# Performance work log

Measured on AMD Instinct MI355X. Metric: run time of the kernel, lower is better.

Reference implementation:

```python
import jax, jax.numpy as jnp
import numpy as np

L = 4      # num_decoders
D = 512    # d (model dim)
F = 512    # f (attention dim; must equal D for residual adds)
V = 32000  # vocab_size
S = 2048   # sequence length
EPS = 1e-5


def layer_norm(x, g, b):
    mu = jnp.mean(x, axis=-1, keepdims=True)
    var = jnp.var(x, axis=-1, keepdims=True)
    return (x - mu) * jax.lax.rsqrt(var + EPS) * g + b


def setup_inputs() -> dict:
    key = jax.random.key(0)
    ks = jax.random.split(key, 20)
    s = 0.02
    n = jax.random.normal
    return {
        "x":   n(ks[0], (S, D), jnp.float32),
        "Wq":  n(ks[1], (L, D, F), jnp.float32) * s,
        "bq":  jnp.zeros((L, F), jnp.float32),
        "Wk":  n(ks[2], (L, D, F), jnp.float32) * s,
        "bk":  jnp.zeros((L, F), jnp.float32),
        "Wv":  n(ks[3], (L, D, F), jnp.float32) * s,
        "bv":  jnp.zeros((L, F), jnp.float32),
        "Wp":  n(ks[4], (L, F, F), jnp.float32) * s,
        "bp":  jnp.zeros((L, F), jnp.float32),
        "g1":  1.0 + n(ks[5], (L, F), jnp.float32) * s,
        "be1": n(ks[6], (L, F), jnp.float32) * s,
        "W1":  n(ks[7], (L, F, 4 * F), jnp.float32) * s,
        "b1":  jnp.zeros((L, 4 * F), jnp.float32),
        "W2":  n(ks[8], (L, 4 * F, D), jnp.float32) * s,
        "b2":  jnp.zeros((L, D), jnp.float32),
        "g2":  1.0 + n(ks[9], (L, D), jnp.float32) * s,
        "be2": n(ks[10], (L, D), jnp.float32) * s,
        "Wf":  n(ks[11], (D, V), jnp.float32) * s,
        "bf":  jnp.zeros((V,), jnp.float32),
    }


def reference(x, Wq, bq, Wk, bk, Wv, bv, Wp, bp, g1, be1, W1, b1, W2, b2, g2, be2, Wf, bf):
    seq = x.shape[0]
    scale = 1.0 / jnp.sqrt(jnp.asarray(F, x.dtype))
    # causal mask: position i attends to j <= i (intended triu masking)
    causal = jnp.tril(jnp.ones((seq, seq), dtype=bool))
    neg_inf = jnp.asarray(-jnp.inf, x.dtype)
    for l in range(L):
        res = jax.lax.stop_gradient(x)  # original uses x.detach().clone()
        q = x @ Wq[l] + bq[l]
        k = x @ Wk[l] + bk[l]
        v = x @ Wv[l] + bv[l]
        scores = (q @ k.T) * scale                      # [S, S]
        scores = jnp.where(causal, scores, neg_inf)
        att = jax.nn.softmax(scores, axis=1)
        z = (att @ v) @ Wp[l] + bp[l]
        x = layer_norm(z + res, g1[l], be1[l])
        res = jax.lax.stop_gradient(x)
        h = x @ W1[l] + b1[l]                           # no activation in original FFN
        h = h @ W2[l] + b2[l]
        x = layer_norm(h + res, g2[l], be2[l])
    logits = x @ Wf + bf                                # [S, V]
    return jax.nn.softmax(logits, axis=1)
```

## Files before the change

kernel.cpp:

```cpp
#include <hip/hip_runtime.h>
#include <cmath>

#define SEQ 2048
#define DIM 512
#define FDIM 512
#define HDIM 2048
#define VOCAB 32000
#define NLAYER 4
#define LNEPS 1e-5f

typedef unsigned short ushort_t;
typedef __attribute__((ext_vector_type(8))) short short8;
typedef __attribute__((ext_vector_type(4))) float f32x4;

__device__ __forceinline__ ushort_t f2bf(float x) {
    union { float f; unsigned int u; } a; a.f = x;
    unsigned int r = a.u + 0x7fffu + ((a.u >> 16) & 1u);
    return (ushort_t)(r >> 16);
}
__device__ __forceinline__ float bf2f(ushort_t b) {
    union { unsigned int u; float f; } a; a.u = ((unsigned int)b) << 16; return a.f;
}

__device__ __forceinline__ void gload_lds16(const ushort_t* g, ushort_t* l) {
    __builtin_amdgcn_global_load_lds(
        (const __attribute__((address_space(1))) void*)g,
        (__attribute__((address_space(3))) void*)l, 16, 0, 0);
}

#define GEMM_CORE(AH, AL, BH, BL, LDA, LDB, KSTEPS, KBASE)                         \
    __shared__ ushort_t lds[16384];                                                \
    ushort_t* ldsAh = lds;                                                         \
    ushort_t* ldsAl = lds + 4096;                                                  \
    ushort_t* ldsBh = lds + 8192;                                                  \
    ushort_t* ldsBl = lds + 12288;                                                 \
    const int tid  = threadIdx.x;                                                  \
    const int lane = tid & 63, wv = tid >> 6;                                      \
    const int wm = wv >> 1, wn = wv & 1;                                           \
    const int q = lane >> 4, mlo = lane & 15;                                      \
    const int tm = blockIdx.y << 7, tn = blockIdx.x << 7;                          \
    f32x4 acc[4][4];                                                               \
    _Pragma("unroll")                                                              \
    for (int i = 0; i < 4; i++)                                                    \
        _Pragma("unroll")                                                          \
        for (int j = 0; j < 4; j++)                                                \
            acc[i][j] = (f32x4){0.f, 0.f, 0.f, 0.f};                               \
    for (int ks = 0; ks < (KSTEPS); ks++) {                                        \
        const int k0 = (KBASE) + (ks << 5);                                        \
        _Pragma("unroll")                                                          \
        for (int r = 0; r < 2; r++) {                                              \
            const int c  = (r << 8) + (wv << 6) + lane;                            \
            const int i  = c & 127, kb = c >> 7;                                   \
            const int lofs = ((r << 8) + (wv << 6)) << 3;                          \
            const size_t aoff = (size_t)(tm + i) * (LDA) + k0 + (kb << 3);         \
            const size_t boff = (size_t)(tn + i) * (LDB) + k0 + (kb << 3);         \
            gload_lds16((AH) + aoff, ldsAh + lofs);                                \
            gload_lds16((AL) + aoff, ldsAl + lofs);                                \
            gload_lds16((BH) + boff, ldsBh + lofs);                                \
            gload_lds16((BL) + boff, ldsBl + lofs);                                \
        }                                                                          \
        __syncthreads();                                                           \
        short8 ah[4], al[4], bh[4], bl[4];                                         \
        _Pragma("unroll")                                                          \
        for (int t = 0; t < 4; t++) {                                              \
            const int ma = ((q << 7) + (wm << 6) + (t << 4) + mlo) << 3;           \
            const int nb = ((q << 7) + (wn << 6) + (t << 4) + mlo) << 3;           \
            ah[t] = *(const short8*)&ldsAh[ma];                                    \
            al[t] = *(const short8*)&ldsAl[ma];                                    \
            bh[t] = *(const short8*)&ldsBh[nb];                                    \
            bl[t] = *(const short8*)&ldsBl[nb];                                    \
        }                                                                          \
        _Pragma("unroll")                                                          \
        for (int i = 0; i < 4; i++)                                                \
            _Pragma("unroll")                                                      \
            for (int j = 0; j < 4; j++) {                                          \
                acc[i][j] = __builtin_amdgcn_mfma_f32_16x16x32_bf16(ah[i], bh[j], acc[i][j], 0, 0, 0); \
                acc[i][j] = __builtin_amdgcn_mfma_f32_16x16x32_bf16(ah[i], bl[j], acc[i][j], 0, 0, 0); \
                acc[i][j] = __builtin_amdgcn_mfma_f32_16x16x32_bf16(al[i], bh[j], acc[i][j], 0, 0, 0); \
            }                                                                      \
        __syncthreads();                                                           \
    }

__global__ __launch_bounds__(256) void gemm_bf16x3_k(
    const ushort_t* __restrict__ Ah, const ushort_t* __restrict__ Al,
    const ushort_t* __restrict__ Bh, const ushort_t* __restrict__ Bl,
    const float* __restrict__ bias, float* __restrict__ C,
    int K, int lda, int ldb, int ldc, float scale, int splitk, int flags,
    int bsA, int bsB, int bsC, int bsBias)
{
    const int bz = blockIdx.z;
    const int l  = bz / splitk, zz = bz - l * splitk;
    Ah += (size_t)l * bsA; Al += (size_t)l * bsA;
    Bh += (size_t)l * bsB; Bl += (size_t)l * bsB;
    C  += (size_t)l * bsC;
    if (bias != nullptr) bias += (size_t)l * bsBias;
    const int tmq = blockIdx.y << 7, tnq = blockIdx.x << 7;
    if ((flags & 1) && tnq > tmq + 127) return;
    int ksteps = (K >> 5) / splitk;
    const int kbase = zz * ksteps * 32;
    if (flags & 2) {
        const int rem = (tmq + 128 - kbase) >> 5;
        if (rem < ksteps) ksteps = rem;
        if (ksteps <= 0) return;
    }
    GEMM_CORE(Ah, Al, Bh, Bl, lda, ldb, ksteps, kbase)
    const bool addb = (bias != nullptr) && (zz == 0);
#pragma unroll
    for (int ti = 0; ti < 4; ti++)
#pragma unroll
        for (int tj = 0; tj < 4; tj++) {
            const int col = tn + (wn << 6) + (tj << 4) + mlo;
            const float bb = addb ? bias[col] : 0.f;
#pragma unroll
            for (int r = 0; r < 4; r++) {
                const int row = tm + (wm << 6) + (ti << 4) + (q << 2) + r;
                const float v = acc[ti][tj][r] * scale + bb;
                if (splitk == 1) C[(size_t)row * ldc + col] = v;
                else atomicAdd(&C[(size_t)row * ldc + col], v);
            }
        }
}

__global__ __launch_bounds__(256) void gemm_bf16x3_sp_k(
    const ushort_t* __restrict__ Ah, const ushort_t* __restrict__ Al,
    const ushort_t* __restrict__ Bh, const ushort_t* __restrict__ Bl,
    const float* __restrict__ bias,
    ushort_t* __restrict__ Dh, ushort_t* __restrict__ Dl,
    int K, int lda, int ldb, int ldo)
{
    GEMM_CORE(Ah, Al, Bh, Bl, lda, ldb, (K >> 5), 0)
#pragma unroll
    for (int ti = 0; ti < 4; ti++)
#pragma unroll
        for (int tj = 0; tj < 4; tj++) {
            const int col = tn + (wn << 6) + (tj << 4) + mlo;
            const float bb = (bias != nullptr) ? bias[col] : 0.f;
#pragma unroll
            for (int r = 0; r < 4; r++) {
                const int row = tm + (wm << 6) + (ti << 4) + (q << 2) + r;
                const float v = acc[ti][tj][r] + bb;
                const ushort_t h = f2bf(v);
                Dh[(size_t)row * ldo + col] = h;
                Dl[(size_t)row * ldo + col] = f2bf(v - bf2f(h));
            }
        }
}

__global__ __launch_bounds__(128) void split_k(
    const float* __restrict__ src, int ld, int C,
    ushort_t* __restrict__ dh, ushort_t* __restrict__ dl)
{
    const int row = blockIdx.y;
    const int c4 = ((blockIdx.x << 7) + threadIdx.x) << 2;
    if (c4 >= C) return;
    const float4 v = *(const float4*)&src[(size_t)row * ld + c4];
    ushort_t h[4], l[4];
    const float f[4] = {v.x, v.y, v.z, v.w};
#pragma unroll
    for (int i = 0; i < 4; i++) {
        h[i] = f2bf(f[i]);
        l[i] = f2bf(f[i] - bf2f(h[i]));
    }
    *(ushort4*)&dh[(size_t)row * C + c4] = make_ushort4(h[0], h[1], h[2], h[3]);
    *(ushort4*)&dl[(size_t)row * C + c4] = make_ushort4(l[0], l[1], l[2], l[3]);
}

__global__ __launch_bounds__(256) void tsplit_k(
    const float* __restrict__ src, int ld, int R,
    ushort_t* __restrict__ dh, ushort_t* __restrict__ dl)
{
    __shared__ float t[32][33];
    const int c = threadIdx.x & 31, r8 = threadIdx.x >> 5;
    const int bx = blockIdx.x, by = blockIdx.y;
#pragma unroll
    for (int i = 0; i < 4; i++) {
        const int r = (r8 << 2) + i;
        t[r][c] = src[(size_t)((by << 5) + r) * ld + (bx << 5) + c];
    }
    __syncthreads();
#pragma unroll
    for (int i = 0; i < 4; i++) {
        const int rr = (r8 << 2) + i;
        const float v = t[c][rr];
        const ushort_t h = f2bf(v);
        const ushort_t l = f2bf(v - bf2f(h));
        const size_t o = (size_t)((bx << 5) + rr) * R + (by << 5) + c;
        dh[o] = h; dl[o] = l;
    }
}

__global__ __launch_bounds__(256) void tsplit_b_k(
    const float* __restrict__ src0, int ld, int R, int sbs,
    ushort_t* __restrict__ dh0, ushort_t* __restrict__ dl0, int dbs)
{
    const int lz = blockIdx.z;
    const float* src = src0 + (size_t)lz * sbs;
    ushort_t* dh = dh0 + (size_t)lz * dbs;
    ushort_t* dl = dl0 + (size_t)lz * dbs;
    __shared__ float t[32][33];
    const int c = threadIdx.x & 31, r8 = threadIdx.x >> 5;
    const int bx = blockIdx.x, by = blockIdx.y;
#pragma unroll
    for (int i = 0; i < 4; i++) {
        const int r = (r8 << 2) + i;
        t[r][c] = src[(size_t)((by << 5) + r) * ld + (bx << 5) + c];
    }
    __syncthreads();
#pragma unroll
    for (int i = 0; i < 4; i++) {
        const int rr = (r8 << 2) + i;
        const float v = t[c][rr];
        const ushort_t h = f2bf(v);
        const ushort_t l = f2bf(v - bf2f(h));
        const size_t o = (size_t)((bx << 5) + rr) * R + (by << 5) + c;
        dh[o] = h; dl[o] = l;
    }
}

__global__ void gatherqkv_k(const float* bq, const float* bk, const float* bv, float* d)
{
    const int i = blockIdx.x * 256 + threadIdx.x;
    if (i >= NLAYER * 1536) return;
    const int l = i / 1536, j = i - l * 1536;
    float v;
    if (j < 512)       v = bq[l * 512 + j];
    else if (j < 1024) v = bk[l * 512 + j - 512];
    else               v = bv[l * 512 + j - 1024];
    d[i] = v;
}

__global__ __launch_bounds__(256) void bvec_k(
    const float* __restrict__ b1, const float* __restrict__ W2,
    float* __restrict__ bv)
{
    const int lz = blockIdx.z;
    b1 += (size_t)lz * HDIM;
    W2 += (size_t)lz * HDIM * DIM;
    bv += (size_t)lz * DIM;
    const int c  = (blockIdx.x << 7) + (threadIdx.x & 127);
    const int h0 = (blockIdx.y << 7) + (threadIdx.x >> 7);
    float acc = 0.f;
#pragma unroll 8
    for (int i = 0; i < 64; i++) {
        const int h = h0 + (i << 1);
        acc += b1[h] * W2[(size_t)h * DIM + c];
    }
    atomicAdd(&bv[c], acc);
}

__global__ __launch_bounds__(256) void softmax_causal_split_k(
    const float* __restrict__ sc, ushort_t* __restrict__ dh, ushort_t* __restrict__ dl)
{
    const int i = blockIdx.x;
    const float* row = sc + (size_t)i * SEQ;
    const int tid = threadIdx.x;
    __shared__ float red[4];
    const int base = tid << 2;

    float4 v[2];
    v[0] = *(const float4*)&row[base];
    v[1] = *(const float4*)&row[1024 + base];

    float m = -3.402823466e38f;
#pragma unroll
    for (int c = 0; c < 2; c++) {
        float* f = (float*)&v[c];
        const int idx = (c << 10) + base;
#pragma unroll
        for (int j = 0; j < 4; j++) {
            if (idx + j > i) f[j] = -3.402823466e38f;
            m = fmaxf(m, f[j]);
        }
    }
#pragma unroll
    for (int o = 32; o > 0; o >>= 1) m = fmaxf(m, __shfl_down(m, o, 64));
    if ((tid & 63) == 0) red[tid >> 6] = m;
    __syncthreads();
    m = fmaxf(fmaxf(red[0], red[1]), fmaxf(red[2], red[3]));
    __syncthreads();

    float s = 0.f;
#pragma unroll
    for (int c = 0; c < 2; c++) {
        float* f = (float*)&v[c];
#pragma unroll
        for (int j = 0; j < 4; j++) {
            f[j] = expf(f[j] - m);
            s += f[j];
        }
    }
#pragma unroll
    for (int o = 32; o > 0; o >>= 1) s += __shfl_down(s, o, 64);
    if ((tid & 63) == 0) red[tid >> 6] = s;
    __syncthreads();
    const float inv = 1.0f / (red[0] + red[1] + red[2] + red[3]);

#pragma unroll
    for (int c = 0; c < 2; c++) {
        float* f = (float*)&v[c];
        const int idx = (c << 10) + base;
        ushort_t hp[4], lp[4];
#pragma unroll
        for (int j = 0; j < 4; j++) {
            const float e = f[j] * inv;
            hp[j] = f2bf(e);
            lp[j] = f2bf(e - bf2f(hp[j]));
        }
        *(ushort4*)&dh[(size_t)i * SEQ + idx] = make_ushort4(hp[0], hp[1], hp[2], hp[3]);
        *(ushort4*)&dl[(size_t)i * SEQ + idx] = make_ushort4(lp[0], lp[1], lp[2], lp[3]);
    }
}

__global__ __launch_bounds__(256) void add_ln_split_k(
    const float* __restrict__ z, const float* __restrict__ res,
    const float* __restrict__ g, const float* __restrict__ b,
    float* __restrict__ outp, ushort_t* __restrict__ dh, ushort_t* __restrict__ dl)
{
    const int row = blockIdx.x;
    const int tid = threadIdx.x;
    __shared__ float red[4];
    const size_t base = (size_t)row * DIM;
    const float v0 = z[base + tid] + res[base + tid];
    const float v1 = z[base + tid + 256] + res[base + tid + 256];
    float s = v0 + v1;
#pragma unroll
    for (int o = 32; o > 0; o >>= 1) s += __shfl_down(s, o, 64);
    if ((tid & 63) == 0) red[tid >> 6] = s;
    __syncthreads();
    const float mean = (red[0] + red[1] + red[2] + red[3]) * (1.0f / DIM);
    __syncthreads();
    const float d0 = v0 - mean, d1 = v1 - mean;
    float vs = d0 * d0 + d1 * d1;
#pragma unroll
    for (int o = 32; o > 0; o >>= 1) vs += __shfl_down(vs, o, 64);
    if ((tid & 63) == 0) red[tid >> 6] = vs;
    __syncthreads();
    const float var = (red[0] + red[1] + red[2] + red[3]) * (1.0f / DIM);
    const float inv = 1.0f / sqrtf(var + LNEPS);
    const float o0 = d0 * inv * g[tid] + b[tid];
    const float o1 = d1 * inv * g[tid + 256] + b[tid + 256];
    outp[base + tid]       = o0;
    outp[base + tid + 256] = o1;
    const ushort_t h0 = f2bf(o0), h1 = f2bf(o1);
    dh[base + tid]       = h0;  dl[base + tid]       = f2bf(o0 - bf2f(h0));
    dh[base + tid + 256] = h1;  dl[base + tid + 256] = f2bf(o1 - bf2f(h1));
}

__global__ __launch_bounds__(1024) void softmax_rows_k(float* __restrict__ p)
{
    const int row = blockIdx.x;
    float* r = p + (size_t)row * VOCAB;
    const int tid = threadIdx.x;
    __shared__ float red[16];
    const int base = tid << 2;

    float4 v[8];
#pragma unroll
    for (int c = 0; c < 7; c++) v[c] = *(const float4*)&r[(c << 12) + base];
    const bool tail = (28672 + base) < VOCAB;
    if (tail) v[7] = *(const float4*)&r[28672 + base];
    else { v[7].x = v[7].y = v[7].z = v[7].w = -3.402823466e38f; }

    float m = -3.402823466e38f;
#pragma unroll
    for (int c = 0; c < 8; c++)
        m = fmaxf(m, fmaxf(fmaxf(v[c].x, v[c].y), fmaxf(v[c].z, v[c].w)));
#pragma unroll
    for (int o = 32; o > 0; o >>= 1) m = fmaxf(m, __shfl_down(m, o, 64));
    if ((tid & 63) == 0) red[tid >> 6] = m;
    __syncthreads();
    m = red[0];
#pragma unroll
    for (int w = 1; w < 16; w++) m = fmaxf(m, red[w]);
    __syncthreads();

    float s = 0.f;
#pragma unroll
    for (int c = 0; c < 8; c++) {
        float* f = (float*)&v[c];
#pragma unroll
        for (int j = 0; j < 4; j++) {
            f[j] = expf(f[j] - m);
            s += f[j];
        }
    }
#pragma unroll
    for (int o = 32; o > 0; o >>= 1) s += __shfl_down(s, o, 64);
    if ((tid & 63) == 0) red[tid >> 6] = s;
    __syncthreads();
    float tot = 0.f;
#pragma unroll
    for (int w = 0; w < 16; w++) tot += red[w];
    const float inv = 1.0f / tot;

#pragma unroll
    for (int c = 0; c < 7; c++) {
        float4 o4;
        o4.x = v[c].x * inv; o4.y = v[c].y * inv;
        o4.z = v[c].z * inv; o4.w = v[c].w * inv;
        *(float4*)&r[(c << 12) + base] = o4;
    }
    if (tail) {
        float4 o4;
        o4.x = v[7].x * inv; o4.y = v[7].y * inv;
        o4.z = v[7].z * inv; o4.w = v[7].w * inv;
        *(float4*)&r[28672 + base] = o4;
    }
}

extern "C" void kernel_launch(void* const* d_in, const int* in_sizes, int n_in,
                              void* d_out, int out_size, void* d_ws, size_t ws_size,
                              hipStream_t stream)
{
    const float* x   = (const float*)d_in[0];
    const float* Wq  = (const float*)d_in[1];
    const float* bq  = (const float*)d_in[2];
    const float* Wk  = (const float*)d_in[3];
    const float* bk  = (const float*)d_in[4];
    const float* Wv  = (const float*)d_in[5];
    const float* bv  = (const float*)d_in[6];
    const float* Wp  = (const float*)d_in[7];
    const float* bp  = (const float*)d_in[8];
    const float* g1  = (const float*)d_in[9];
    const float* be1 = (const float*)d_in[10];
    const float* W1  = (const float*)d_in[11];
    const float* b1  = (const float*)d_in[12];
    const float* W2  = (const float*)d_in[13];
    const float* b2  = (const float*)d_in[14];
    const float* g2  = (const float*)d_in[15];
    const float* be2 = (const float*)d_in[16];
    const float* Wf  = (const float*)d_in[17];
    const float* bf  = (const float*)d_in[18];
    float* out = (float*)d_out;

    char* ws = (char*)d_ws;
    auto alloc = [&](size_t bytes) {
        void* p = ws;
        ws += (bytes + 255) & ~(size_t)255;
        return p;
    };
    float*    x0     = (float*)alloc((size_t)SEQ * DIM * 4);
    float*    x1     = (float*)alloc((size_t)SEQ * DIM * 4);
    float*    vp     = (float*)alloc((size_t)SEQ * FDIM * 4);
    float*    z2     = (float*)alloc((size_t)SEQ * FDIM * 4);
    float*    sc     = (float*)alloc((size_t)SEQ * SEQ * 4);
    float*    PtA    = (float*)alloc((size_t)NLAYER * FDIM * DIM * 4);
    ushort_t* QKVh   = (ushort_t*)alloc((size_t)SEQ * 1536 * 2);
    ushort_t* QKVl   = (ushort_t*)alloc((size_t)SEQ * 1536 * 2);
    ushort_t* X0h    = (ushort_t*)alloc((size_t)SEQ * DIM * 2);
    ushort_t* X0l    = (ushort_t*)alloc((size_t)SEQ * DIM * 2);
    ushort_t* X1h    = (ushort_t*)alloc((size_t)SEQ * DIM * 2);
    ushort_t* X1l    = (ushort_t*)alloc((size_t)SEQ * DIM * 2);
    ushort_t* AttH   = (ushort_t*)alloc((size_t)SEQ * SEQ * 2);
    ushort_t* AttL   = (ushort_t*)alloc((size_t)SEQ * SEQ * 2);
    ushort_t* Wbh    = (ushort_t*)alloc((size_t)NLAYER * 1536 * 512 * 2);
    ushort_t* Wbl    = (ushort_t*)alloc((size_t)NLAYER * 1536 * 512 * 2);
    ushort_t* WpTh   = (ushort_t*)alloc((size_t)NLAYER * 512 * 512 * 2);
    ushort_t* WpTl   = (ushort_t*)alloc((size_t)NLAYER * 512 * 512 * 2);
    ushort_t* W2th   = (ushort_t*)alloc((size_t)NLAYER * 512 * 2048 * 2);
    ushort_t* W2tl   = (ushort_t*)alloc((size_t)NLAYER * 512 * 2048 * 2);
    ushort_t* W1h    = (ushort_t*)alloc((size_t)NLAYER * 512 * 2048 * 2);
    ushort_t* W1l    = (ushort_t*)alloc((size_t)NLAYER * 512 * 2048 * 2);
    ushort_t* Pth    = (ushort_t*)alloc((size_t)NLAYER * 512 * 512 * 2);
    ushort_t* Ptl    = (ushort_t*)alloc((size_t)NLAYER * 512 * 512 * 2);
    ushort_t* VpTh   = (ushort_t*)alloc((size_t)FDIM * SEQ * 2);
    ushort_t* VpTl   = (ushort_t*)alloc((size_t)FDIM * SEQ * 2);
    ushort_t* Wfh    = (ushort_t*)alloc((size_t)VOCAB * DIM * 2);
    ushort_t* Wfl    = (ushort_t*)alloc((size_t)VOCAB * DIM * 2);
    float*    bqkvA  = (float*)alloc((size_t)NLAYER * 1536 * 4);
    float*    bvecA  = (float*)alloc((size_t)NLAYER * DIM * 4);

    const float att_scale = 1.0f / sqrtf((float)FDIM);
    const dim3 b256(256), b128(128), b1024(1024);

    auto split = [&](const float* src, int ld, int R, int C, ushort_t* dh, ushort_t* dl) {
        split_k<<<dim3((C / 4 + 127) / 128, R), b128, 0, stream>>>(src, ld, C, dh, dl);
    };
    auto gemm = [&](const ushort_t* ah, const ushort_t* al,
                    const ushort_t* bh, const ushort_t* bl,
                    const float* bias, float* C, int M, int N, int K,
                    int lda, int ldb, int ldc, float scale, int splitk, int flags) {
        if (splitk > 1)
            hipMemsetAsync(C, 0, (size_t)M * ldc * 4, stream);
        gemm_bf16x3_k<<<dim3(N / 128, M / 128, splitk), b256, 0, stream>>>(
            ah, al, bh, bl, bias, C, K, lda, ldb, ldc, scale, splitk, flags, 0, 0, 0, 0);
    };

    hipMemcpyAsync(x0, x, (size_t)SEQ * DIM * 4, hipMemcpyDeviceToDevice, stream);
    tsplit_b_k<<<dim3(16, 16, NLAYER), b256, 0, stream>>>(Wq, FDIM, DIM, 262144, Wbh, Wbl, 786432);
    tsplit_b_k<<<dim3(16, 16, NLAYER), b256, 0, stream>>>(Wk, FDIM, DIM, 262144, Wbh + 262144, Wbl + 262144, 786432);
    tsplit_b_k<<<dim3(16, 16, NLAYER), b256, 0, stream>>>(Wv, FDIM, DIM, 262144, Wbh + 524288, Wbl + 524288, 786432);
    tsplit_b_k<<<dim3(16, 16, NLAYER), b256, 0, stream>>>(Wp, FDIM, FDIM, 262144, WpTh, WpTl, 262144);
    tsplit_b_k<<<dim3(16, 64, NLAYER), b256, 0, stream>>>(W2, DIM, HDIM, HDIM * DIM, W2th, W2tl, 1048576);
    split(W1, HDIM, NLAYER * FDIM, HDIM, W1h, W1l);
    hipMemsetAsync(PtA, 0, (size_t)NLAYER * FDIM * DIM * 4, stream);
    gemm_bf16x3_k<<<dim3(4, 4, NLAYER * 8), b256, 0, stream>>>(
        W2th, W2tl, W1h, W1l, nullptr, PtA, HDIM, HDIM, HDIM, DIM, 1.0f, 8, 0,
        1048576, 1048576, 262144, 0);
    split(PtA, DIM, NLAYER * FDIM, DIM, Pth, Ptl);
    gatherqkv_k<<<dim3((NLAYER * 1536 + 255) / 256), b256, 0, stream>>>(bq, bk, bv, bqkvA);
    hipMemcpyAsync(bvecA, b2, (size_t)NLAYER * DIM * 4, hipMemcpyDeviceToDevice, stream);
    bvec_k<<<dim3(4, 16, NLAYER), b256, 0, stream>>>(b1, W2, bvecA);
    tsplit_k<<<dim3(VOCAB / 32, DIM / 32), b256, 0, stream>>>(Wf, VOCAB, DIM, Wfh, Wfl);
    split(x0, DIM, SEQ, DIM, X0h, X0l);

    for (int l = 0; l < NLAYER; l++) {
        gemm_bf16x3_sp_k<<<dim3(12, 16), b256, 0, stream>>>(
            X0h, X0l, Wbh + (size_t)l * 786432, Wbl + (size_t)l * 786432,
            bqkvA + (size_t)l * 1536, QKVh, QKVl, DIM, DIM, DIM, 1536);

        gemm(QKVh + 1024, QKVl + 1024, WpTh + (size_t)l * 262144, WpTl + (size_t)l * 262144,
             nullptr, vp, SEQ, FDIM, FDIM, 1536, FDIM, FDIM, 1.0f, 4, 0);

        gemm(QKVh, QKVl, QKVh + 512, QKVl + 512, nullptr, sc,
             SEQ, SEQ, FDIM, 1536, 1536, SEQ, att_scale, 2, 1);
        softmax_causal_split_k<<<dim3(SEQ), b256, 0, stream>>>(sc, AttH, AttL);

        tsplit_k<<<dim3(16, 64), b256, 0, stream>>>(vp, FDIM, SEQ, VpTh, VpTl);
        gemm(AttH, AttL, VpTh, VpTl, bp + l * FDIM, z2,
             SEQ, FDIM, SEQ, SEQ, SEQ, FDIM, 1.0f, 4, 2);

        add_ln_split_k<<<dim3(SEQ), b256, 0, stream>>>(
            z2, x0, g1 + l * FDIM, be1 + l * FDIM, x1, X1h, X1l);

        gemm(X1h, X1l, Pth + (size_t)l * 262144, Ptl + (size_t)l * 262144,
             bvecA + (size_t)l * DIM, z2, SEQ, DIM, FDIM, DIM, DIM, DIM, 1.0f, 4, 0);

        add_ln_split_k<<<dim3(SEQ), b256, 0, stream>>>(
            z2, x1, g2 + l * DIM, be2 + l * DIM, x0, X0h, X0l);
    }

    gemm_bf16x3_k<<<dim3(VOCAB / 128, SEQ / 128, 1), b256, 0, stream>>>(
        X0h, X0l, Wfh, Wfl, bf, out, DIM, DIM, DIM, VOCAB, 1.0f, 1, 0, 0, 0, 0, 0);
    softmax_rows_k<<<dim3(SEQ), b1024, 0, stream>>>(out);
}
```

Baseline: 1.687 ms.

## Fold Wv into Wp, replace atomic split-K with partial buffers, swizzle vocab GEMM

Precomputes Wv·Wp (and bv·Wp) once, so the V projection goes straight into a transposed layout. This removes the per-layer vp GEMM and the transpose-split kernel. Split-K GEMMs now write separate partial buffers that the softmax and add+layernorm kernels sum, which drops the memsets and atomics. Partial sums that are causally empty are skipped. Softmax stores only the columns inside the causal limit, and the final vocab GEMM swaps block indices so consecutive blocks share weight tiles. The cost is more memory traffic for the partial buffers and a slightly different rounding order.

After: 1.514 ms. 10.3% less time.

```diff
diff --git a/kernel.cpp b/kernel.cpp
--- a/kernel.cpp
+++ b/kernel.cpp
@@ -28,7 +28,7 @@
         (__attribute__((address_space(3))) void*)l, 16, 0, 0);
 }
 
-#define GEMM_CORE(AH, AL, BH, BL, LDA, LDB, KSTEPS, KBASE)                         \
+#define GEMM_CORE(AH, AL, BH, BL, LDA, LDB, KSTEPS, KBASE, TM, TN)                 \
     __shared__ ushort_t lds[16384];                                                \
     ushort_t* ldsAh = lds;                                                         \
     ushort_t* ldsAl = lds + 4096;                                                  \
@@ -38,7 +38,7 @@
     const int lane = tid & 63, wv = tid >> 6;                                      \
     const int wm = wv >> 1, wn = wv & 1;                                           \
     const int q = lane >> 4, mlo = lane & 15;                                      \
-    const int tm = blockIdx.y << 7, tn = blockIdx.x << 7;                          \
+    const int tm = (TM), tn = (TN);                                                \
     f32x4 acc[4][4];                                                               \
     _Pragma("unroll")                                                              \
     for (int i = 0; i < 4; i++)                                                    \
@@ -86,7 +86,7 @@
     const ushort_t* __restrict__ Bh, const ushort_t* __restrict__ Bl,
     const float* __restrict__ bias, float* __restrict__ C,
     int K, int lda, int ldb, int ldc, float scale, int splitk, int flags,
-    int bsA, int bsB, int bsC, int bsBias)
+    int bsA, int bsB, int bsC, int bsBias, int bsPart)
 {
     const int bz = blockIdx.z;
     const int l  = bz / splitk, zz = bz - l * splitk;
@@ -94,7 +94,9 @@
     Bh += (size_t)l * bsB; Bl += (size_t)l * bsB;
     C  += (size_t)l * bsC;
     if (bias != nullptr) bias += (size_t)l * bsBias;
-    const int tmq = blockIdx.y << 7, tnq = blockIdx.x << 7;
+    int bx = blockIdx.x, by = blockIdx.y;
+    if (flags & 4) { const int t = bx; bx = by; by = t; }
+    const int tmq = by << 7, tnq = bx << 7;
     if ((flags & 1) && tnq > tmq + 127) return;
     int ksteps = (K >> 5) / splitk;
     const int kbase = zz * ksteps * 32;
@@ -103,8 +105,9 @@
         if (rem < ksteps) ksteps = rem;
         if (ksteps <= 0) return;
     }
-    GEMM_CORE(Ah, Al, Bh, Bl, lda, ldb, ksteps, kbase)
+    GEMM_CORE(Ah, Al, Bh, Bl, lda, ldb, ksteps, kbase, tmq, tnq)
     const bool addb = (bias != nullptr) && (zz == 0);
+    float* Cw = C + ((splitk > 1 && bsPart) ? (size_t)zz * bsPart : 0);
 #pragma unroll
     for (int ti = 0; ti < 4; ti++)
 #pragma unroll
@@ -115,33 +118,40 @@
             for (int r = 0; r < 4; r++) {
                 const int row = tm + (wm << 6) + (ti << 4) + (q << 2) + r;
                 const float v = acc[ti][tj][r] * scale + bb;
-                if (splitk == 1) C[(size_t)row * ldc + col] = v;
+                if (splitk == 1 || bsPart) Cw[(size_t)row * ldc + col] = v;
                 else atomicAdd(&C[(size_t)row * ldc + col], v);
             }
         }
 }
 
-__global__ __launch_bounds__(256) void gemm_bf16x3_sp_k(
+__global__ __launch_bounds__(256) void gemm_qkv_k(
     const ushort_t* __restrict__ Ah, const ushort_t* __restrict__ Al,
     const ushort_t* __restrict__ Bh, const ushort_t* __restrict__ Bl,
     const float* __restrict__ bias,
-    ushort_t* __restrict__ Dh, ushort_t* __restrict__ Dl,
-    int K, int lda, int ldb, int ldo)
-{
-    GEMM_CORE(Ah, Al, Bh, Bl, lda, ldb, (K >> 5), 0)
+    ushort_t* __restrict__ QKh, ushort_t* __restrict__ QKl,
+    ushort_t* __restrict__ Vh,  ushort_t* __restrict__ Vl)
+{
+    GEMM_CORE(Ah, Al, Bh, Bl, DIM, DIM, (DIM >> 5), 0,
+              (int)(blockIdx.y << 7), (int)(blockIdx.x << 7))
 #pragma unroll
     for (int ti = 0; ti < 4; ti++)
 #pragma unroll
         for (int tj = 0; tj < 4; tj++) {
             const int col = tn + (wn << 6) + (tj << 4) + mlo;
-            const float bb = (bias != nullptr) ? bias[col] : 0.f;
+            const float bb = bias[col];
 #pragma unroll
             for (int r = 0; r < 4; r++) {
                 const int row = tm + (wm << 6) + (ti << 4) + (q << 2) + r;
                 const float v = acc[ti][tj][r] + bb;
                 const ushort_t h = f2bf(v);
-                Dh[(size_t)row * ldo + col] = h;
-                Dl[(size_t)row * ldo + col] = f2bf(v - bf2f(h));
+                const ushort_t lo = f2bf(v - bf2f(h));
+                if (col < 1024) {
+                    QKh[(size_t)row * 1024 + col] = h;
+                    QKl[(size_t)row * 1024 + col] = lo;
+                } else {
+                    Vh[(size_t)(col - 1024) * SEQ + row] = h;
+                    Vl[(size_t)(col - 1024) * SEQ + row] = lo;
+                }
             }
         }
 }
@@ -150,6 +160,29 @@
     const float* __restrict__ src, int ld, int C,
     ushort_t* __restrict__ dh, ushort_t* __restrict__ dl)
 {
+    const int row = blockIdx.y;
+    const int c4 = ((blockIdx.x << 7) + threadIdx.x) << 2;
+    if (c4 >= C) return;
+    const float4 v = *(const float4*)&src[(size_t)row * ld + c4];
+    ushort_t h[4], l[4];
+    const float f[4] = {v.x, v.y, v.z, v.w};
+#pragma unroll
+    for (int i = 0; i < 4; i++) {
+        h[i] = f2bf(f[i]);
+        l[i] = f2bf(f[i] - bf2f(h[i]));
+    }
+    *(ushort4*)&dh[(size_t)row * C + c4] = make_ushort4(h[0], h[1], h[2], h[3]);
+    *(ushort4*)&dl[(size_t)row * C + c4] = make_ushort4(l[0], l[1], l[2], l[3]);
+}
+
+__global__ __launch_bounds__(128) void split_b_k(
+    const float* __restrict__ src0, int ld, int C, int sbs,
+    ushort_t* __restrict__ dh0, ushort_t* __restrict__ dl0, int dbs)
+{
+    const int lz = blockIdx.z;
+    const float* src = src0 + (size_t)lz * sbs;
+    ushort_t* dh = dh0 + (size_t)lz * dbs;
+    ushort_t* dl = dl0 + (size_t)lz * dbs;
     const int row = blockIdx.y;
     const int c4 = ((blockIdx.x << 7) + threadIdx.x) << 2;
     if (c4 >= C) return;
@@ -217,7 +250,7 @@
     }
 }
 
-__global__ void gatherqkv_k(const float* bq, const float* bk, const float* bv, float* d)
+__global__ void gatherqkv_k(const float* bq, const float* bk, const float* bvp, float* d)
 {
     const int i = blockIdx.x * 256 + threadIdx.x;
     if (i >= NLAYER * 1536) return;
@@ -225,41 +258,49 @@
     float v;
     if (j < 512)       v = bq[l * 512 + j];
     else if (j < 1024) v = bk[l * 512 + j - 512];
-    else               v = bv[l * 512 + j - 1024];
+    else               v = bvp[l * 512 + j - 1024];
     d[i] = v;
 }
 
-__global__ __launch_bounds__(256) void bvec_k(
-    const float* __restrict__ b1, const float* __restrict__ W2,
-    float* __restrict__ bv)
+__global__ __launch_bounds__(256) void bvecg_k(
+    const float* __restrict__ vec, const float* __restrict__ W,
+    float* __restrict__ outp, int sbsV, int sbsW)
 {
     const int lz = blockIdx.z;
-    b1 += (size_t)lz * HDIM;
-    W2 += (size_t)lz * HDIM * DIM;
-    bv += (size_t)lz * DIM;
+    vec  += (size_t)lz * sbsV;
+    W    += (size_t)lz * sbsW;
+    outp += (size_t)lz * DIM;
     const int c  = (blockIdx.x << 7) + (threadIdx.x & 127);
     const int h0 = (blockIdx.y << 7) + (threadIdx.x >> 7);
     float acc = 0.f;
 #pragma unroll 8
     for (int i = 0; i < 64; i++) {
         const int h = h0 + (i << 1);
-        acc += b1[h] * W2[(size_t)h * DIM + c];
-    }
-    atomicAdd(&bv[c], acc);
+        acc += vec[h] * W[(size_t)h * DIM + c];
+    }
+    atomicAdd(&outp[c], acc);
 }
 
 __global__ __launch_bounds__(256) void softmax_causal_split_k(
     const float* __restrict__ sc, ushort_t* __restrict__ dh, ushort_t* __restrict__ dl)
 {
     const int i = blockIdx.x;
-    const float* row = sc + (size_t)i * SEQ;
+    const float* p0 = sc + (size_t)i * SEQ;
+    const float* p1 = p0 + (size_t)SEQ * SEQ;
     const int tid = threadIdx.x;
     __shared__ float red[4];
     const int base = tid << 2;
+    const int lim = ((i >> 7) + 1) << 7;
 
     float4 v[2];
-    v[0] = *(const float4*)&row[base];
-    v[1] = *(const float4*)&row[1024 + base];
+#pragma unroll
+    for (int c = 0; c < 2; c++) {
+        const int idx = (c << 10) + base;
+        const float4 a = *(const float4*)&p0[idx];
+        const float4 b = *(const float4*)&p1[idx];
+        v[c].x = a.x + b.x; v[c].y = a.y + b.y;
+        v[c].z = a.z + b.z; v[c].w = a.w + b.w;
+    }
 
     float m = -3.402823466e38f;
 #pragma unroll
@@ -299,6 +340,7 @@
     for (int c = 0; c < 2; c++) {
         float* f = (float*)&v[c];
         const int idx = (c << 10) + base;
+        if (idx >= lim) continue;
         ushort_t hp[4], lp[4];
 #pragma unroll
         for (int j = 0; j < 4; j++) {
@@ -312,16 +354,24 @@
 }
 
 __global__ __launch_bounds__(256) void add_ln_split_k(
-    const float* __restrict__ z, const float* __restrict__ res,
+    const float* __restrict__ zp, const float* __restrict__ res,
     const float* __restrict__ g, const float* __restrict__ b,
-    float* __restrict__ outp, ushort_t* __restrict__ dh, ushort_t* __restrict__ dl)
+    float* __restrict__ outp, ushort_t* __restrict__ dh, ushort_t* __restrict__ dl,
+    int parts, int clampk)
 {
     const int row = blockIdx.x;
     const int tid = threadIdx.x;
     __shared__ float red[4];
     const size_t base = (size_t)row * DIM;
-    const float v0 = z[base + tid] + res[base + tid];
-    const float v1 = z[base + tid + 256] + res[base + tid + 256];
+    const size_t pst  = (size_t)SEQ * DIM;
+    int np = clampk ? ((row >> 9) + 1) : parts;
+    if (np > parts) np = parts;
+    float v0 = res[base + tid];
+    float v1 = res[base + tid + 256];
+    for (int p = 0; p < np; p++) {
+        v0 += zp[(size_t)p * pst + base + tid];
+        v1 += zp[(size_t)p * pst + base + tid + 256];
+    }
     float s = v0 + v1;
 #pragma unroll
     for (int o = 32; o > 0; o >>= 1) s += __shfl_down(s, o, 64);
@@ -441,12 +491,12 @@
     };
     float*    x0     = (float*)alloc((size_t)SEQ * DIM * 4);
     float*    x1     = (float*)alloc((size_t)SEQ * DIM * 4);
-    float*    vp     = (float*)alloc((size_t)SEQ * FDIM * 4);
-    float*    z2     = (float*)alloc((size_t)SEQ * FDIM * 4);
-    float*    sc     = (float*)alloc((size_t)SEQ * SEQ * 4);
+    float*    z2p    = (float*)alloc((size_t)4 * SEQ * DIM * 4);
+    float*    sc     = (float*)alloc((size_t)2 * SEQ * SEQ * 4);
     float*    PtA    = (float*)alloc((size_t)NLAYER * FDIM * DIM * 4);
-    ushort_t* QKVh   = (ushort_t*)alloc((size_t)SEQ * 1536 * 2);
-    ushort_t* QKVl   = (ushort_t*)alloc((size_t)SEQ * 1536 * 2);
+    float*    WvpA   = (float*)alloc((size_t)NLAYER * FDIM * DIM * 4);
+    ushort_t* QKh    = (ushort_t*)alloc((size_t)SEQ * 1024 * 2);
+    ushort_t* QKl    = (ushort_t*)alloc((size_t)SEQ * 1024 * 2);
     ushort_t* X0h    = (ushort_t*)alloc((size_t)SEQ * DIM * 2);
     ushort_t* X0l    = (ushort_t*)alloc((size_t)SEQ * DIM * 2);
     ushort_t* X1h    = (ushort_t*)alloc((size_t)SEQ * DIM * 2);
@@ -457,6 +507,8 @@
     ushort_t* Wbl    = (ushort_t*)alloc((size_t)NLAYER * 1536 * 512 * 2);
     ushort_t* WpTh   = (ushort_t*)alloc((size_t)NLAYER * 512 * 512 * 2);
     ushort_t* WpTl   = (ushort_t*)alloc((size_t)NLAYER * 512 * 512 * 2);
+    ushort_t* Wvh    = (ushort_t*)alloc((size_t)NLAYER * 512 * 512 * 2);
+    ushort_t* Wvl    = (ushort_t*)alloc((size_t)NLAYER * 512 * 512 * 2);
     ushort_t* W2th   = (ushort_t*)alloc((size_t)NLAYER * 512 * 2048 * 2);
     ushort_t* W2tl   = (ushort_t*)alloc((size_t)NLAYER * 512 * 2048 * 2);
     ushort_t* W1h    = (ushort_t*)alloc((size_t)NLAYER * 512 * 2048 * 2);
@@ -468,69 +520,67 @@
     ushort_t* Wfh    = (ushort_t*)alloc((size_t)VOCAB * DIM * 2);
     ushort_t* Wfl    = (ushort_t*)alloc((size_t)VOCAB * DIM * 2);
     float*    bqkvA  = (float*)alloc((size_t)NLAYER * 1536 * 4);
+    float*    bvpA   = (float*)alloc((size_t)NLAYER * DIM * 4);
     float*    bvecA  = (float*)alloc((size_t)NLAYER * DIM * 4);
 
     const float att_scale = 1.0f / sqrtf((float)FDIM);
     const dim3 b256(256), b128(128), b1024(1024);
-
-    auto split = [&](const float* src, int ld, int R, int C, ushort_t* dh, ushort_t* dl) {
-        split_k<<<dim3((C / 4 + 127) / 128, R), b128, 0, stream>>>(src, ld, C, dh, dl);
-    };
-    auto gemm = [&](const ushort_t* ah, const ushort_t* al,
-                    const ushort_t* bh, const ushort_t* bl,
-                    const float* bias, float* C, int M, int N, int K,
-                    int lda, int ldb, int ldc, float scale, int splitk, int flags) {
-        if (splitk > 1)
-            hipMemsetAsync(C, 0, (size_t)M * ldc * 4, stream);
-        gemm_bf16x3_k<<<dim3(N / 128, M / 128, splitk), b256, 0, stream>>>(
-            ah, al, bh, bl, bias, C, K, lda, ldb, ldc, scale, splitk, flags, 0, 0, 0, 0);
-    };
 
     hipMemcpyAsync(x0, x, (size_t)SEQ * DIM * 4, hipMemcpyDeviceToDevice, stream);
     tsplit_b_k<<<dim3(16, 16, NLAYER), b256, 0, stream>>>(Wq, FDIM, DIM, 262144, Wbh, Wbl, 786432);
     tsplit_b_k<<<dim3(16, 16, NLAYER), b256, 0, stream>>>(Wk, FDIM, DIM, 262144, Wbh + 262144, Wbl + 262144, 786432);
-    tsplit_b_k<<<dim3(16, 16, NLAYER), b256, 0, stream>>>(Wv, FDIM, DIM, 262144, Wbh + 524288, Wbl + 524288, 786432);
     tsplit_b_k<<<dim3(16, 16, NLAYER), b256, 0, stream>>>(Wp, FDIM, FDIM, 262144, WpTh, WpTl, 262144);
+    split_k<<<dim3(1, NLAYER * 512), b128, 0, stream>>>(Wv, 512, 512, Wvh, Wvl);
+    hipMemsetAsync(WvpA, 0, (size_t)NLAYER * FDIM * DIM * 4, stream);
+    gemm_bf16x3_k<<<dim3(4, 4, NLAYER * 2), b256, 0, stream>>>(
+        WpTh, WpTl, Wvh, Wvl, nullptr, WvpA, 512, 512, 512, 512, 1.0f, 2, 0,
+        262144, 262144, 262144, 0, 0);
+    split_b_k<<<dim3(1, 512, NLAYER), b128, 0, stream>>>(
+        WvpA, 512, 512, 262144, Wbh + 524288, Wbl + 524288, 786432);
+    hipMemsetAsync(bvpA, 0, (size_t)NLAYER * DIM * 4, stream);
+    bvecg_k<<<dim3(4, 4, NLAYER), b256, 0, stream>>>(bv, Wp, bvpA, 512, 262144);
     tsplit_b_k<<<dim3(16, 64, NLAYER), b256, 0, stream>>>(W2, DIM, HDIM, HDIM * DIM, W2th, W2tl, 1048576);
-    split(W1, HDIM, NLAYER * FDIM, HDIM, W1h, W1l);
+    split_k<<<dim3(4, NLAYER * 512), b128, 0, stream>>>(W1, HDIM, HDIM, W1h, W1l);
     hipMemsetAsync(PtA, 0, (size_t)NLAYER * FDIM * DIM * 4, stream);
     gemm_bf16x3_k<<<dim3(4, 4, NLAYER * 8), b256, 0, stream>>>(
         W2th, W2tl, W1h, W1l, nullptr, PtA, HDIM, HDIM, HDIM, DIM, 1.0f, 8, 0,
-        1048576, 1048576, 262144, 0);
-    split(PtA, DIM, NLAYER * FDIM, DIM, Pth, Ptl);
-    gatherqkv_k<<<dim3((NLAYER * 1536 + 255) / 256), b256, 0, stream>>>(bq, bk, bv, bqkvA);
+        1048576, 1048576, 262144, 0, 0);
+    split_k<<<dim3(1, NLAYER * 512), b128, 0, stream>>>(PtA, DIM, DIM, Pth, Ptl);
     hipMemcpyAsync(bvecA, b2, (size_t)NLAYER * DIM * 4, hipMemcpyDeviceToDevice, stream);
-    bvec_k<<<dim3(4, 16, NLAYER), b256, 0, stream>>>(b1, W2, bvecA);
+    bvecg_k<<<dim3(4, 16, NLAYER), b256, 0, stream>>>(b1, W2, bvecA, HDIM, HDIM * DIM);
+    gatherqkv_k<<<dim3(24), b256, 0, stream>>>(bq, bk, bvpA, bqkvA);
     tsplit_k<<<dim3(VOCAB / 32, DIM / 32), b256, 0, stream>>>(Wf, VOCAB, DIM, Wfh, Wfl);
-    split(x0, DIM, SEQ, DIM, X0h, X0l);
+    split_k<<<dim3(1, SEQ), b128, 0, stream>>>(x0, DIM, DIM, X0h, X0l);
 
     for (int l = 0; l < NLAYER; l++) {
-        gemm_bf16x3_sp_k<<<dim3(12, 16), b256, 0, stream>>>(
+        gemm_qkv_k<<<dim3(12, 16), b256, 0, stream>>>(
             X0h, X0l, Wbh + (size_t)l * 786432, Wbl + (size_t)l * 786432,
-            bqkvA + (size_t)l * 1536, QKVh, QKVl, DIM, DIM, DIM, 1536);
-
-        gemm(QKVh + 1024, QKVl + 1024, WpTh + (size_t)l * 262144, WpTl + (size_t)l * 262144,
-             nullptr, vp, SEQ, FDIM, FDIM, 1536, FDIM, FDIM, 1.0f, 4, 0);
-
-        gemm(QKVh, QKVl, QKVh + 512, QKVl + 512, nullptr, sc,
-             SEQ, SEQ, FDIM, 1536, 1536, SEQ, att_scale, 2, 1);
+            bqkvA + (size_t)l * 1536, QKh, QKl, VpTh, VpTl);
+
+        gemm_bf16x3_k<<<dim3(16, 16, 2), b256, 0, stream>>>(
+            QKh, QKl, QKh + 512, QKl + 512, nullptr, sc,
+            FDIM, 1024, 1024, SEQ, att_scale, 2, 1, 0, 0, 0, 0, SEQ * SEQ);
+
         softmax_causal_split_k<<<dim3(SEQ), b256, 0, stream>>>(sc, AttH, AttL);
 
-        tsplit_k<<<dim3(16, 64), b256, 0, stream>>>(vp, FDIM, SEQ, VpTh, VpTl);
-        gemm(AttH, AttL, VpTh, VpTl, bp + l * FDIM, z2,
-             SEQ, FDIM, SEQ, SEQ, SEQ, FDIM, 1.0f, 4, 2);
+        gemm_bf16x3_k<<<dim3(4, 16, 4), b256, 0, stream>>>(
+            AttH, AttL, VpTh, VpTl, bp + l * FDIM, z2p,
+            SEQ, SEQ, SEQ, DIM, 1.0f, 4, 2, 0, 0, 0, 0, SEQ * DIM);
 
         add_ln_split_k<<<dim3(SEQ), b256, 0, stream>>>(
-            z2, x0, g1 + l * FDIM, be1 + l * FDIM, x1, X1h, X1l);
-
-        gemm(X1h, X1l, Pth + (size_t)l * 262144, Ptl + (size_t)l * 262144,
-             bvecA + (size_t)l * DIM, z2, SEQ, DIM, FDIM, DIM, DIM, DIM, 1.0f, 4, 0);
+            z2p, x0, g1 + l * FDIM, be1 + l * FDIM, x1, X1h, X1l, 4, 1);
+
+        gemm_bf16x3_k<<<dim3(4, 16, 4), b256, 0, stream>>>(
+            X1h, X1l, Pth + (size_t)l * 262144, Ptl + (size_t)l * 262144,
+            bvecA + (size_t)l * DIM, z2p, DIM, DIM, DIM, DIM, 1.0f, 4, 0,
+            0, 0, 0, 0, SEQ * DIM);
 
         add_ln_split_k<<<dim3(SEQ), b256, 0, stream>>>(
-            z2, x1, g2 + l * DIM, be2 + l * DIM, x0, X0h, X0l);
-    }
-
-    gemm_bf16x3_k<<<dim3(VOCAB / 128, SEQ / 128, 1), b256, 0, stream>>>(
-        X0h, X0l, Wfh, Wfl, bf, out, DIM, DIM, DIM, VOCAB, 1.0f, 1, 0, 0, 0, 0, 0);
+            z2p, x1, g2 + l * DIM, be2 + l * DIM, x0, X0h, X0l, 4, 0);
+    }
+
+    gemm_bf16x3_k<<<dim3(SEQ / 128, VOCAB / 128, 1), b256, 0, stream>>>(
+        X0h, X0l, Wfh, Wfl, bf, out, DIM, DIM, DIM, VOCAB, 1.0f, 1, 4,
+        0, 0, 0, 0, 0);
     softmax_rows_k<<<dim3(SEQ), b1024, 0, stream>>>(out);
 }
```
